# Optimization experiments

Hardware: AMD Instinct MI355X
Metric: run time of the kernel (lower is better)

The kernel has to match this reference:

```python
import jax, jax.numpy as jnp
import numpy as np

N = 4096
IN_DIM = 6
HID = 32
HEADS1 = 4
OUT_DIM = 64


def _gat_layer(x, mask, W, a_src, a_dst, b):
    # x: [n, in], W: [in, heads*d], a_src/a_dst: [heads, d], b: [heads*d]
    n = x.shape[0]
    heads, d = a_src.shape
    h = (x @ W).reshape(n, heads, d)                      # [n, heads, d]
    e_src = jnp.einsum('nhd,hd->nh', h, a_src)            # [n, heads]
    e_dst = jnp.einsum('nhd,hd->nh', h, a_dst)            # [n, heads]
    logits = e_src[:, None, :] + e_dst[None, :, :]        # [n, n, heads]
    logits = jax.nn.leaky_relu(logits, negative_slope=0.2)
    logits = jnp.where(mask[:, :, None], logits, jnp.float32(-1e9))
    alpha = jax.nn.softmax(logits, axis=1)                # softmax over j (dim=1)
    # dropout disabled (eval mode reference)
    out = jnp.einsum('ijh,jhd->ihd', alpha, h).reshape(n, heads * d)
    return out + b


def setup_inputs() -> dict:
    key = jax.random.key(0)
    ks = jax.random.split(key, 10)
    x = jax.random.normal(ks[0], (N, IN_DIM), dtype=jnp.float32)
    adj = jax.random.bernoulli(ks[1], 0.01, (N, N)).astype(jnp.float32)
    s = 0.1
    W1 = jax.random.normal(ks[2], (IN_DIM, HEADS1 * HID), dtype=jnp.float32) * s
    a_src1 = jax.random.normal(ks[3], (HEADS1, HID), dtype=jnp.float32) * s
    a_dst1 = jax.random.normal(ks[4], (HEADS1, HID), dtype=jnp.float32) * s
    b1 = jnp.zeros((HEADS1 * HID,), dtype=jnp.float32)
    W2 = jax.random.normal(ks[5], (HEADS1 * HID, OUT_DIM), dtype=jnp.float32) * s
    a_src2 = jax.random.normal(ks[6], (1, OUT_DIM), dtype=jnp.float32) * s
    a_dst2 = jax.random.normal(ks[7], (1, OUT_DIM), dtype=jnp.float32) * s
    b2 = jnp.zeros((OUT_DIM,), dtype=jnp.float32)
    return {'x': x, 'adj': adj, 'W1': W1, 'a_src1': a_src1, 'a_dst1': a_dst1,
            'b1': b1, 'W2': W2, 'a_src2': a_src2, 'a_dst2': a_dst2, 'b2': b2}


def reference(x, adj, W1, a_src1, a_dst1, b1, W2, a_src2, a_dst2, b2):
    n = x.shape[0]
    # add self loops: a = max(a, I), mask = a > 0
    a = jnp.maximum(adj, jnp.eye(n, dtype=adj.dtype))
    mask = a > 0
    h1 = jax.nn.elu(_gat_layer(x, mask, W1, a_src1, a_dst1, b1))
    # dropout disabled (eval mode)
    h2 = _gat_layer(h1, mask, W2, a_src2, a_dst2, b2)
    return h2
```

## Files before the change

### kernel.cpp

```cpp
#include <hip/hip_runtime.h>

#define N 4096
#define IN_DIM 6
#define HID 32
#define HEADS1 4
#define D1 (HEADS1*HID)
#define OUT_DIM 64
#define MAXNB 192

__global__ void kA(const float* __restrict__ x,
                   const float* __restrict__ W1,
                   const float* __restrict__ a_src1,
                   const float* __restrict__ a_dst1,
                   float* __restrict__ hpre,
                   float* __restrict__ es1,
                   float* __restrict__ ed1) {
    int t  = threadIdx.x;
    int r  = t >> 7;
    int tt = t & 127;
    int i  = blockIdx.x * 2 + r;
    __shared__ float xs[2][IN_DIM];
    if (tt < IN_DIM) xs[r][tt] = x[i*IN_DIM + tt];
    __syncthreads();
    float acc = 0.f;
    #pragma unroll
    for (int k = 0; k < IN_DIM; ++k)
        acc += xs[r][k] * W1[k*D1 + tt];
    hpre[(size_t)i*D1 + tt] = acc;
    float ps = acc * a_src1[tt];
    float pd = acc * a_dst1[tt];
    #pragma unroll
    for (int off = 16; off >= 1; off >>= 1) {
        ps += __shfl_xor(ps, off, 64);
        pd += __shfl_xor(pd, off, 64);
    }
    if ((tt & 31) == 0) {
        int h = tt >> 5;
        es1[i*HEADS1 + h] = ps;
        ed1[i*HEADS1 + h] = pd;
    }
}

__global__ __launch_bounds__(512) void kB(
                   const float* __restrict__ adj,
                   const float* __restrict__ hpre,
                   const float* __restrict__ es1,
                   const float* __restrict__ ed1,
                   const float* __restrict__ b1,
                   const float* __restrict__ W2,
                   const float* __restrict__ a_src2,
                   const float* __restrict__ a_dst2,
                   int* __restrict__ cnt, int* __restrict__ idxg,
                   float* __restrict__ h2pre,
                   float* __restrict__ es2, float* __restrict__ ed2) {
    int i = blockIdx.x;
    int t = threadIdx.x;
    __shared__ int   cL;
    __shared__ int   js[MAXNB];
    __shared__ float lg[HEADS1][MAXNB];
    __shared__ float esi[HEADS1];
    __shared__ float sinv[HEADS1];
    __shared__ float part[3][D1];
    __shared__ float h1s[D1];
    __shared__ float p2s[512];
    if (t == 0) cL = 0;
    if (t < HEADS1) esi[t] = es1[i*HEADS1 + t];
    __syncthreads();

    const float4* row = (const float4*)(adj + (size_t)i * N);
    float4 v0 = row[t];
    float4 v1 = row[t + 512];
    float f[8] = {v0.x, v0.y, v0.z, v0.w, v1.x, v1.y, v1.z, v1.w};
    #pragma unroll
    for (int q = 0; q < 8; ++q) {
        int j = (q < 4) ? (t*4 + q) : (2048 + t*4 + (q - 4));
        if (f[q] > 0.f || j == i) {
            int p = atomicAdd(&cL, 1);
            if (p < MAXNB) js[p] = j;
        }
    }
    __syncthreads();
    int c = min(cL, MAXNB);

    if (t < c) {
        int j = js[t];
        float4 e4 = ((const float4*)ed1)[j];
        float l0 = esi[0] + e4.x, l1 = esi[1] + e4.y,
              l2 = esi[2] + e4.z, l3 = esi[3] + e4.w;
        lg[0][t] = (l0 > 0.f) ? l0 : 0.2f*l0;
        lg[1][t] = (l1 > 0.f) ? l1 : 0.2f*l1;
        lg[2][t] = (l2 > 0.f) ? l2 : 0.2f*l2;
        lg[3][t] = (l3 > 0.f) ? l3 : 0.2f*l3;
    }
    if (t >= 256) {
        int p = t - 256;
        if (p == 0) cnt[i] = c;
        if (p < c) idxg[i*MAXNB + p] = js[p];
    }
    __syncthreads();

    if (t < 256) {
        int h = t >> 6, l = t & 63;
        float m = -1e30f;
        for (int p = l; p < c; p += 64) m = fmaxf(m, lg[h][p]);
        #pragma unroll
        for (int off = 32; off >= 1; off >>= 1) m = fmaxf(m, __shfl_xor(m, off, 64));
        float s = 0.f;
        for (int p = l; p < c; p += 64) {
            float e = __expf(lg[h][p] - m);
            lg[h][p] = e;
            s += e;
        }
        #pragma unroll
        for (int off = 32; off >= 1; off >>= 1) s += __shfl_xor(s, off, 64);
        if (l == 0) sinv[h] = 1.f / s;
    }
    __syncthreads();

    int g = t >> 7, tt = t & 127, hh = tt >> 5;
    float acc = 0.f;
    int p = g;
    for (; p + 12 < c; p += 16) {
        int   j0 = js[p],      j1 = js[p+4],   j2 = js[p+8],   j3 = js[p+12];
        float w0 = lg[hh][p],  w1 = lg[hh][p+4], w2 = lg[hh][p+8], w3 = lg[hh][p+12];
        float x0 = hpre[(size_t)j0*D1 + tt];
        float x1 = hpre[(size_t)j1*D1 + tt];
        float x2 = hpre[(size_t)j2*D1 + tt];
        float x3 = hpre[(size_t)j3*D1 + tt];
        acc += w0*x0 + w1*x1 + w2*x2 + w3*x3;
    }
    for (; p < c; p += 4)
        acc += lg[hh][p] * hpre[(size_t)js[p]*D1 + tt];
    if (g) part[g-1][tt] = acc;
    __syncthreads();
    if (g == 0) {
        acc += part[0][tt] + part[1][tt] + part[2][tt];
        float val = acc * sinv[hh] + b1[tt];
        h1s[tt] = (val > 0.f) ? val : expm1f(val);
    }
    __syncthreads();

    int o = t & 63, q = t >> 6;
    float pa = 0.f;
    #pragma unroll
    for (int k = 0; k < 16; ++k) {
        int kk = q*16 + k;
        pa += h1s[kk] * W2[kk*OUT_DIM + o];
    }
    p2s[t] = pa;
    __syncthreads();
    if (t < 64) {
        float h2 = 0.f;
        #pragma unroll
        for (int qq = 0; qq < 8; ++qq) h2 += p2s[t + 64*qq];
        h2pre[(size_t)i*OUT_DIM + t] = h2;
        float ps = h2 * a_src2[t];
        float pd = h2 * a_dst2[t];
        #pragma unroll
        for (int off = 32; off >= 1; off >>= 1) {
            ps += __shfl_xor(ps, off, 64);
            pd += __shfl_xor(pd, off, 64);
        }
        if (t == 0) { es2[i] = ps; ed2[i] = pd; }
    }
}

__global__ __launch_bounds__(256) void kC(
                   const float* __restrict__ h2pre,
                   const float* __restrict__ es2,
                   const float* __restrict__ ed2,
                   const int* __restrict__ cnt,
                   const int* __restrict__ idxg,
                   const float* __restrict__ b2v,
                   float* __restrict__ out) {
    int i = blockIdx.x;
    int t = threadIdx.x;
    int c = cnt[i];
    __shared__ int   js[MAXNB];
    __shared__ float al[MAXNB];
    __shared__ float sinv_s;
    __shared__ float part[3][OUT_DIM];
    float esi = es2[i];
    if (t < c) {
        int j = idxg[i*MAXNB + t];
        js[t] = j;
        float l = esi + ed2[j];
        al[t] = (l > 0.f) ? l : 0.2f*l;
    }
    __syncthreads();
    if (t < 64) {
        float m = -1e30f;
        for (int p = t; p < c; p += 64) m = fmaxf(m, al[p]);
        #pragma unroll
        for (int off = 32; off >= 1; off >>= 1) m = fmaxf(m, __shfl_xor(m, off, 64));
        float s = 0.f;
        for (int p = t; p < c; p += 64) {
            float e = __expf(al[p] - m);
            al[p] = e;
            s += e;
        }
        #pragma unroll
        for (int off = 32; off >= 1; off >>= 1) s += __shfl_xor(s, off, 64);
        if (t == 0) sinv_s = 1.f / s;
    }
    __syncthreads();
    int g = t >> 6, o = t & 63;
    float acc = 0.f;
    int p = g;
    for (; p + 12 < c; p += 16) {
        int   j0 = js[p],    j1 = js[p+4],  j2 = js[p+8],  j3 = js[p+12];
        float w0 = al[p],    w1 = al[p+4],  w2 = al[p+8],  w3 = al[p+12];
        float x0 = h2pre[(size_t)j0*OUT_DIM + o];
        float x1 = h2pre[(size_t)j1*OUT_DIM + o];
        float x2 = h2pre[(size_t)j2*OUT_DIM + o];
        float x3 = h2pre[(size_t)j3*OUT_DIM + o];
        acc += w0*x0 + w1*x1 + w2*x2 + w3*x3;
    }
    for (; p < c; p += 4)
        acc += al[p] * h2pre[(size_t)js[p]*OUT_DIM + o];
    if (g) part[g-1][o] = acc;
    __syncthreads();
    if (g == 0) {
        acc += part[0][o] + part[1][o] + part[2][o];
        out[(size_t)i*OUT_DIM + o] = acc * sinv_s + b2v[o];
    }
}

extern "C" void kernel_launch(void* const* d_in, const int* in_sizes, int n_in,
                              void* d_out, int out_size, void* d_ws, size_t ws_size,
                              hipStream_t stream) {
    const float* x      = (const float*)d_in[0];
    const float* adj    = (const float*)d_in[1];
    const float* W1     = (const float*)d_in[2];
    const float* a_src1 = (const float*)d_in[3];
    const float* a_dst1 = (const float*)d_in[4];
    const float* b1     = (const float*)d_in[5];
    const float* W2     = (const float*)d_in[6];
    const float* a_src2 = (const float*)d_in[7];
    const float* a_dst2 = (const float*)d_in[8];
    const float* b2v    = (const float*)d_in[9];
    float* out = (float*)d_out;

    float* ws    = (float*)d_ws;
    float* hpre  = ws;
    float* h2pre = hpre  + (size_t)N*D1;
    float* es1   = h2pre + (size_t)N*OUT_DIM;
    float* ed1   = es1   + (size_t)N*HEADS1;
    float* es2   = ed1   + (size_t)N*HEADS1;
    float* ed2   = es2   + N;
    int*   cnt   = (int*)(ed2 + N);
    int*   idxg  = cnt + N;

    kA<<<N/2, 256, 0, stream>>>(x, W1, a_src1, a_dst1, hpre, es1, ed1);
    kB<<<N,   512, 0, stream>>>(adj, hpre, es1, ed1, b1, W2, a_src2, a_dst2,
                                cnt, idxg, h2pre, es2, ed2);
    kC<<<N,   256, 0, stream>>>(h2pre, es2, ed2, cnt, idxg, b2v, out);
}
```

Before: 137.1 us.

## Fuse three GAT kernels into one cooperative persistent kernel with grid syncs

Replaces the three separate launches with a single cooperative kernel of 512 blocks of 256 threads. Each block handles 8 rows per phase, and grid.sync separates the phases. The adjacency row for the next node is prefetched while the current one is processed, and the softmax exponentials are recomputed inside the aggregation loop instead of being written back to shared memory. This is meant to cut launch overhead and tail effects, at the cost of fewer threads per row, grid-wide barriers, and a fallback path to the old kernels when cooperative launch is unavailable.

```diff
diff --git a/kernel.cpp b/kernel.cpp
--- a/kernel.cpp
+++ b/kernel.cpp
@@ -1,4 +1,7 @@
 #include <hip/hip_runtime.h>
+#include <hip/hip_cooperative_groups.h>
+
+namespace cg = cooperative_groups;
 
 #define N 4096
 #define IN_DIM 6
@@ -7,14 +10,226 @@
 #define D1 (HEADS1*HID)
 #define OUT_DIM 64
 #define MAXNB 192
-
-__global__ void kA(const float* __restrict__ x,
-                   const float* __restrict__ W1,
-                   const float* __restrict__ a_src1,
-                   const float* __restrict__ a_dst1,
-                   float* __restrict__ hpre,
-                   float* __restrict__ es1,
-                   float* __restrict__ ed1) {
+#define GRIDC 512
+#define ROWS 8
+
+__global__ __launch_bounds__(256, 4) void kfused(
+    const float* __restrict__ x,
+    const float* __restrict__ adj,
+    const float* __restrict__ W1,
+    const float* __restrict__ a_src1,
+    const float* __restrict__ a_dst1,
+    const float* __restrict__ b1,
+    const float* __restrict__ W2,
+    const float* __restrict__ a_src2,
+    const float* __restrict__ a_dst2,
+    const float* __restrict__ b2v,
+    float* __restrict__ hpre,  float* __restrict__ es1, float* __restrict__ ed1,
+    float* __restrict__ h2pre, float* __restrict__ es2, float* __restrict__ ed2,
+    int* __restrict__ cnt,     int* __restrict__ idxg,  float* __restrict__ out)
+{
+    cg::grid_group grid = cg::this_grid();
+    int t   = threadIdx.x;
+    int blk = blockIdx.x;
+
+    {
+        __shared__ float xs[2][IN_DIM];
+        int r2 = t >> 7;
+        int tt = t & 127;
+        for (int pr = 0; pr < ROWS/2; ++pr) {
+            int i = blk*ROWS + pr*2 + r2;
+            if (tt < IN_DIM) xs[r2][tt] = x[i*IN_DIM + tt];
+            __syncthreads();
+            float acc = 0.f;
+            #pragma unroll
+            for (int k = 0; k < IN_DIM; ++k)
+                acc += xs[r2][k] * W1[k*D1 + tt];
+            hpre[(size_t)i*D1 + tt] = acc;
+            float ps = acc * a_src1[tt];
+            float pd = acc * a_dst1[tt];
+            #pragma unroll
+            for (int off = 16; off >= 1; off >>= 1) {
+                ps += __shfl_xor(ps, off, 64);
+                pd += __shfl_xor(pd, off, 64);
+            }
+            if ((tt & 31) == 0) {
+                int h = tt >> 5;
+                es1[i*HEADS1 + h] = ps;
+                ed1[i*HEADS1 + h] = pd;
+            }
+            __syncthreads();
+        }
+    }
+    grid.sync();
+
+    {
+        __shared__ int   cS;
+        __shared__ int   js[MAXNB];
+        __shared__ float lg[HEADS1][MAXNB];
+        __shared__ float esiS[HEADS1];
+        __shared__ float part[D1];
+        __shared__ float h1s[D1];
+        __shared__ float p2s[256];
+
+        const float4* row0 = (const float4*)(adj + (size_t)(blk*ROWS) * N);
+        float4 v0 = row0[t], v1 = row0[t+256], v2 = row0[t+512], v3 = row0[t+768];
+
+        for (int pr = 0; pr < ROWS; ++pr) {
+            int i = blk*ROWS + pr;
+            if (t == 0) cS = 0;
+            if (t < HEADS1) esiS[t] = es1[i*HEADS1 + t];
+            __syncthreads();
+
+            {
+                float4 vv[4] = {v0, v1, v2, v3};
+                #pragma unroll
+                for (int ch = 0; ch < 4; ++ch) {
+                    float ff[4] = {vv[ch].x, vv[ch].y, vv[ch].z, vv[ch].w};
+                    #pragma unroll
+                    for (int q = 0; q < 4; ++q) {
+                        int j = (t + 256*ch)*4 + q;
+                        if (ff[q] > 0.f || j == i) {
+                            int p = atomicAdd(&cS, 1);
+                            if (p < MAXNB) js[p] = j;
+                        }
+                    }
+                }
+            }
+            __syncthreads();
+            int c = min(cS, MAXNB);
+
+            if (pr + 1 < ROWS) {
+                const float4* rn = (const float4*)(adj + (size_t)(i+1) * N);
+                v0 = rn[t]; v1 = rn[t+256]; v2 = rn[t+512]; v3 = rn[t+768];
+            }
+
+            if (t < c) {
+                int j = js[t];
+                float4 e4 = ((const float4*)ed1)[j];
+                float l0 = esiS[0] + e4.x, l1 = esiS[1] + e4.y,
+                      l2 = esiS[2] + e4.z, l3 = esiS[3] + e4.w;
+                lg[0][t] = (l0 > 0.f) ? l0 : 0.2f*l0;
+                lg[1][t] = (l1 > 0.f) ? l1 : 0.2f*l1;
+                lg[2][t] = (l2 > 0.f) ? l2 : 0.2f*l2;
+                lg[3][t] = (l3 > 0.f) ? l3 : 0.2f*l3;
+                idxg[i*MAXNB + t] = j;
+            }
+            if (t == 0) cnt[i] = c;
+            __syncthreads();
+
+            int g = t >> 7, tt = t & 127, hh = tt >> 5, hl = t & 31;
+            float m = -1e30f;
+            for (int p = hl; p < c; p += 32) m = fmaxf(m, lg[hh][p]);
+            #pragma unroll
+            for (int off = 16; off >= 1; off >>= 1) m = fmaxf(m, __shfl_xor(m, off, 64));
+            float s = 0.f;
+            for (int p = hl; p < c; p += 32) s += __expf(lg[hh][p] - m);
+            #pragma unroll
+            for (int off = 16; off >= 1; off >>= 1) s += __shfl_xor(s, off, 64);
+            float inv = 1.f / s;
+
+            float acc = 0.f;
+            int p = g;
+            for (; p + 6 < c; p += 8) {
+                int   j0 = js[p],   j1 = js[p+2], j2 = js[p+4], j3 = js[p+6];
+                float w0 = __expf(lg[hh][p]   - m), w1 = __expf(lg[hh][p+2] - m),
+                      w2 = __expf(lg[hh][p+4] - m), w3 = __expf(lg[hh][p+6] - m);
+                float x0 = hpre[(size_t)j0*D1 + tt];
+                float x1 = hpre[(size_t)j1*D1 + tt];
+                float x2 = hpre[(size_t)j2*D1 + tt];
+                float x3 = hpre[(size_t)j3*D1 + tt];
+                acc += w0*x0 + w1*x1 + w2*x2 + w3*x3;
+            }
+            for (; p < c; p += 2)
+                acc += __expf(lg[hh][p] - m) * hpre[(size_t)js[p]*D1 + tt];
+            if (g == 1) part[tt] = acc;
+            __syncthreads();
+            if (g == 0) {
+                acc += part[tt];
+                float val = acc * inv + b1[tt];
+                h1s[tt] = (val > 0.f) ? val : expm1f(val);
+            }
+            __syncthreads();
+
+            int o = t & 63, q = t >> 6;
+            float pa = 0.f;
+            #pragma unroll
+            for (int k = 0; k < 32; ++k) {
+                int kk = q*32 + k;
+                pa += h1s[kk] * W2[kk*OUT_DIM + o];
+            }
+            p2s[t] = pa;
+            __syncthreads();
+            if (t < 64) {
+                float h2 = p2s[t] + p2s[t+64] + p2s[t+128] + p2s[t+192];
+                h2pre[(size_t)i*OUT_DIM + t] = h2;
+                float ps = h2 * a_src2[t];
+                float pd = h2 * a_dst2[t];
+                #pragma unroll
+                for (int off = 32; off >= 1; off >>= 1) {
+                    ps += __shfl_xor(ps, off, 64);
+                    pd += __shfl_xor(pd, off, 64);
+                }
+                if (t == 0) { es2[i] = ps; ed2[i] = pd; }
+            }
+            __syncthreads();
+        }
+    }
+    grid.sync();
+
+    {
+        __shared__ int   jsC[MAXNB];
+        __shared__ float al[MAXNB];
+        __shared__ float partC[3][OUT_DIM];
+        for (int pr = 0; pr < ROWS; ++pr) {
+            int i = blk*ROWS + pr;
+            int c = cnt[i];
+            float esi = es2[i];
+            if (t < c) {
+                int j = idxg[i*MAXNB + t];
+                jsC[t] = j;
+                float l = esi + ed2[j];
+                al[t] = (l > 0.f) ? l : 0.2f*l;
+            }
+            __syncthreads();
+            int l6 = t & 63;
+            float m = -1e30f;
+            for (int p = l6; p < c; p += 64) m = fmaxf(m, al[p]);
+            #pragma unroll
+            for (int off = 32; off >= 1; off >>= 1) m = fmaxf(m, __shfl_xor(m, off, 64));
+            float s = 0.f;
+            for (int p = l6; p < c; p += 64) s += __expf(al[p] - m);
+            #pragma unroll
+            for (int off = 32; off >= 1; off >>= 1) s += __shfl_xor(s, off, 64);
+            float inv = 1.f / s;
+            int g = t >> 6, o = l6;
+            float acc = 0.f;
+            int p = g;
+            for (; p + 12 < c; p += 16) {
+                int   j0 = jsC[p],  j1 = jsC[p+4], j2 = jsC[p+8], j3 = jsC[p+12];
+                float w0 = __expf(al[p]    - m), w1 = __expf(al[p+4]  - m),
+                      w2 = __expf(al[p+8]  - m), w3 = __expf(al[p+12] - m);
+                float x0 = h2pre[(size_t)j0*OUT_DIM + o];
+                float x1 = h2pre[(size_t)j1*OUT_DIM + o];
+                float x2 = h2pre[(size_t)j2*OUT_DIM + o];
+                float x3 = h2pre[(size_t)j3*OUT_DIM + o];
+                acc += w0*x0 + w1*x1 + w2*x2 + w3*x3;
+            }
+            for (; p < c; p += 4)
+                acc += __expf(al[p] - m) * h2pre[(size_t)jsC[p]*OUT_DIM + o];
+            if (g) partC[g-1][o] = acc;
+            __syncthreads();
+            if (g == 0)
+                out[(size_t)i*OUT_DIM + o] =
+                    (acc + partC[0][o] + partC[1][o] + partC[2][o]) * inv + b2v[o];
+            __syncthreads();
+        }
+    }
+}
+
+__global__ void kA_fb(const float* __restrict__ x, const float* __restrict__ W1,
+                      const float* __restrict__ a_src1, const float* __restrict__ a_dst1,
+                      float* __restrict__ hpre, float* __restrict__ es1, float* __restrict__ ed1) {
     int t  = threadIdx.x;
     int r  = t >> 7;
     int tt = t & 127;
@@ -24,8 +239,7 @@
     __syncthreads();
     float acc = 0.f;
     #pragma unroll
-    for (int k = 0; k < IN_DIM; ++k)
-        acc += xs[r][k] * W1[k*D1 + tt];
+    for (int k = 0; k < IN_DIM; ++k) acc += xs[r][k] * W1[k*D1 + tt];
     hpre[(size_t)i*D1 + tt] = acc;
     float ps = acc * a_src1[tt];
     float pd = acc * a_dst1[tt];
@@ -41,18 +255,13 @@
     }
 }
 
-__global__ __launch_bounds__(512) void kB(
-                   const float* __restrict__ adj,
-                   const float* __restrict__ hpre,
-                   const float* __restrict__ es1,
-                   const float* __restrict__ ed1,
-                   const float* __restrict__ b1,
-                   const float* __restrict__ W2,
-                   const float* __restrict__ a_src2,
-                   const float* __restrict__ a_dst2,
+__global__ __launch_bounds__(512) void kB_fb(
+                   const float* __restrict__ adj, const float* __restrict__ hpre,
+                   const float* __restrict__ es1, const float* __restrict__ ed1,
+                   const float* __restrict__ b1,  const float* __restrict__ W2,
+                   const float* __restrict__ a_src2, const float* __restrict__ a_dst2,
                    int* __restrict__ cnt, int* __restrict__ idxg,
-                   float* __restrict__ h2pre,
-                   float* __restrict__ es2, float* __restrict__ ed2) {
+                   float* __restrict__ h2pre, float* __restrict__ es2, float* __restrict__ ed2) {
     int i = blockIdx.x;
     int t = threadIdx.x;
     __shared__ int   cL;
@@ -66,7 +275,6 @@
     if (t == 0) cL = 0;
     if (t < HEADS1) esi[t] = es1[i*HEADS1 + t];
     __syncthreads();
-
     const float4* row = (const float4*)(adj + (size_t)i * N);
     float4 v0 = row[t];
     float4 v1 = row[t + 512];
@@ -81,12 +289,10 @@
     }
     __syncthreads();
     int c = min(cL, MAXNB);
-
     if (t < c) {
         int j = js[t];
         float4 e4 = ((const float4*)ed1)[j];
-        float l0 = esi[0] + e4.x, l1 = esi[1] + e4.y,
-              l2 = esi[2] + e4.z, l3 = esi[3] + e4.w;
+        float l0 = esi[0] + e4.x, l1 = esi[1] + e4.y, l2 = esi[2] + e4.z, l3 = esi[3] + e4.w;
         lg[0][t] = (l0 > 0.f) ? l0 : 0.2f*l0;
         lg[1][t] = (l1 > 0.f) ? l1 : 0.2f*l1;
         lg[2][t] = (l2 > 0.f) ? l2 : 0.2f*l2;
@@ -98,7 +304,6 @@
         if (p < c) idxg[i*MAXNB + p] = js[p];
     }
     __syncthreads();
-
     if (t < 256) {
         int h = t >> 6, l = t & 63;
         float m = -1e30f;
@@ -116,7 +321,6 @@
         if (l == 0) sinv[h] = 1.f / s;
     }
     __syncthreads();
-
     int g = t >> 7, tt = t & 127, hh = tt >> 5;
     float acc = 0.f;
     int p = g;
@@ -139,7 +343,6 @@
         h1s[tt] = (val > 0.f) ? val : expm1f(val);
     }
     __syncthreads();
-
     int o = t & 63, q = t >> 6;
     float pa = 0.f;
     #pragma unroll
@@ -165,13 +368,10 @@
     }
 }
 
-__global__ __launch_bounds__(256) void kC(
-                   const float* __restrict__ h2pre,
-                   const float* __restrict__ es2,
-                   const float* __restrict__ ed2,
-                   const int* __restrict__ cnt,
-                   const int* __restrict__ idxg,
-                   const float* __restrict__ b2v,
+__global__ __launch_bounds__(256) void kC_fb(
+                   const float* __restrict__ h2pre, const float* __restrict__ es2,
+                   const float* __restrict__ ed2, const int* __restrict__ cnt,
+                   const int* __restrict__ idxg, const float* __restrict__ b2v,
                    float* __restrict__ out) {
     int i = blockIdx.x;
     int t = threadIdx.x;
@@ -251,8 +451,32 @@
     int*   cnt   = (int*)(ed2 + N);
     int*   idxg  = cnt + N;
 
-    kA<<<N/2, 256, 0, stream>>>(x, W1, a_src1, a_dst1, hpre, es1, ed1);
-    kB<<<N,   512, 0, stream>>>(adj, hpre, es1, ed1, b1, W2, a_src2, a_dst2,
-                                cnt, idxg, h2pre, es2, ed2);
-    kC<<<N,   256, 0, stream>>>(h2pre, es2, ed2, cnt, idxg, b2v, out);
+    static int use_coop = -1;
+    if (use_coop < 0) {
+        int dev = 0, attr = 0, ncu = 0, perCU = 0;
+        hipGetDevice(&dev);
+        hipDeviceGetAttribute(&attr, hipDeviceAttributeCooperativeLaunch, dev);
+        hipDeviceGetAttribute(&ncu, hipDeviceAttributeMultiprocessorCount, dev);
+        hipOccupancyMaxActiveBlocksPerMultiprocessor(&perCU, kfused, 256, 0);
+        use_coop = (attr && (long)perCU * ncu >= GRIDC) ? 1 : 0;
+    }
+
+    if (use_coop) {
+        void* args[] = {
+            (void*)&x, (void*)&adj, (void*)&W1, (void*)&a_src1, (void*)&a_dst1,
+            (void*)&b1, (void*)&W2, (void*)&a_src2, (void*)&a_dst2, (void*)&b2v,
+            (void*)&hpre, (void*)&es1, (void*)&ed1,
+            (void*)&h2pre, (void*)&es2, (void*)&ed2,
+            (void*)&cnt, (void*)&idxg, (void*)&out
+        };
+        hipError_t e = hipLaunchCooperativeKernel((void*)kfused, dim3(GRIDC), dim3(256),
+                                                  args, 0, stream);
+        if (e == hipSuccess) return;
+        use_coop = 0;
+    }
+
+    kA_fb<<<N/2, 256, 0, stream>>>(x, W1, a_src1, a_dst1, hpre, es1, ed1);
+    kB_fb<<<N,   512, 0, stream>>>(adj, hpre, es1, ed1, b1, W2, a_src2, a_dst2,
+                                   cnt, idxg, h2pre, es2, ed2);
+    kC_fb<<<N,   256, 0, stream>>>(h2pre, es2, ed2, cnt, idxg, b2v, out);
 }
```

Result: slower. 286.0 us (+108.6%).
